# Optimization experiments

Hardware: AMD Instinct MI355X
Metric: run time of the kernel (lower is better)

Reference implementation:

```python
import jax, jax.numpy as jnp
import numpy as np

N_CHANNELS = 256
N_NEIGHBOURS = 262144
DIM = 3


def setup_inputs() -> dict:
    key = jax.random.key(0)
    k1, k2, k3 = jax.random.split(key, 3)
    h = jax.random.normal(k1, (N_CHANNELS, N_NEIGHBOURS), dtype=jnp.float32)
    rel_poss = jax.random.normal(k2, (DIM, N_NEIGHBOURS), dtype=jnp.float32)
    W = jax.random.normal(k3, (N_CHANNELS, N_CHANNELS), dtype=jnp.float32)
    return {"h": h, "rel_poss": rel_poss, "W": W}


def reference(h, rel_poss, W):
    # dists: [N], unit directions u: [dim, N]
    dists = jnp.linalg.norm(rel_poss, axis=0)
    u = rel_poss / dists
    # radial basis e_rbf(x, n, c=2) = (2/2)**0.5 * sin(n*x)/x = sin(n*x)/x, n = 1..K
    n = jnp.arange(1, N_CHANNELS + 1, dtype=h.dtype)
    radial_emb = jnp.sin(n[:, None] * dists[None, :]) / dists[None, :]  # [K, N]
    # channel-mixed features
    hp = W @ h  # [K, N]
    # per-neighbour: radial * feature scalar times rank-2 outer product u u^T, summed over neighbours
    m = radial_emb * hp  # [K, N]
    A = jnp.einsum('ki,di,ei->kde', m, u, u)  # [K, dim, dim]
    return A
```

## Files before the change

kernel.cpp:

```cpp
#include <hip/hip_runtime.h>
#include <hip/hip_bf16.h>

#define NCH      256
#define NNB      262144
#define BN       64
#define NTILES   (NNB / BN)
#define NB       256
#define ITPB     (NTILES / NB)
#define NENT     (NCH * 6)

typedef __bf16        bf16x8 __attribute__((ext_vector_type(8)));
typedef float         f32x4  __attribute__((ext_vector_type(4)));
typedef unsigned int  u32x4  __attribute__((ext_vector_type(4)));
typedef unsigned int  u32x2  __attribute__((ext_vector_type(2)));
typedef short         v4s    __attribute__((ext_vector_type(4)));

union FragU  { u32x4 u; bf16x8 b; };
union Frag2U { u32x2 u; v4s    s; };

__device__ __forceinline__ unsigned pk2(float lo, float hi) {
    union { __hip_bfloat162 h2; unsigned u; } cv;
    cv.h2 = __float22bfloat162_rn(make_float2(lo, hi));
    return cv.u;
}

__device__ __forceinline__ const float* uni_ptr(const float* p) {
    unsigned long long u = (unsigned long long)p;
    unsigned lo = __builtin_amdgcn_readfirstlane((unsigned)u);
    unsigned hi = __builtin_amdgcn_readfirstlane((unsigned)(u >> 32));
    return (const float*)(((unsigned long long)hi << 32) | lo);
}

#define LBAR() do {                                                  \
    asm volatile("s_waitcnt lgkmcnt(0)" ::: "memory");               \
    __builtin_amdgcn_sched_barrier(0);                               \
    __builtin_amdgcn_s_barrier();                                    \
    __builtin_amdgcn_sched_barrier(0);                               \
} while (0)

#define ITER(P, CUR, NXT, TILE_EXPR)                                               \
{                                                                                  \
    const int tile = (TILE_EXPR);                                                  \
    const int tn1  = tile + NB;                                                    \
    const int tn2  = tile + 2 * NB;                                                \
    {                      \
        const int lt = (tn2 < NTILES) ? tn2 : tile;                                \
        const unsigned ii = (unsigned)(lt * BN) + (unsigned)c;                     \
        NXT[0] = rp[ii];                                                           \
        NXT[1] = rp[(size_t)NNB + ii];                                             \
        NXT[2] = rp[2 * (size_t)NNB + ii];                                         \
    }                                                                              \
    __builtin_amdgcn_sched_barrier(0);                                             \
                      \
    _Pragma("unroll")                                                              \
    for (int cb = 0; cb < 4; ++cb) {                                               \
        const int colb = cb * 16;                                                  \
        Frag2U gf;                                                                 \
        gf.u = *(const u32x2*)((const char*)gT[P] +                                \
               (((unsigned)(il * 128 + (colb + q * 4) * 2)) ^                      \
                (((unsigned)(il & 7)) << 3)));                                     \
        f32x4 hpA = {0.f, 0.f, 0.f, 0.f}, hpB = {0.f, 0.f, 0.f, 0.f};              \
        const unsigned rb = (unsigned)((colb + il) * 512);                         \
        const unsigned sw = ((unsigned)(il & 7)) << 4;                             \
        _Pragma("unroll")                                                          \
        for (int jb = 0; jb < 8; jb += 2) {                                        \
            FragU f0, f1;                                                          \
            f0.u = *(const u32x4*)((const char*)htile[P] +                         \
                   ((rb + (unsigned)(jb * 64 + q * 16)) ^ sw));                    \
            f1.u = *(const u32x4*)((const char*)htile[P] +                         \
                   ((rb + (unsigned)((jb + 1) * 64 + q * 16)) ^ sw));              \
            hpA = __builtin_amdgcn_mfma_f32_16x16x32_bf16(f0.b, wf[jb].b, hpA, 0, 0, 0);     \
            hpB = __builtin_amdgcn_mfma_f32_16x16x32_bf16(f1.b, wf[jb + 1].b, hpB, 0, 0, 0); \
        }                                                                          \
        f32x4 d4 = *(const f32x4*)&dtab[P][0][colb + q * 4];                       \
        f32x4 i4 = *(const f32x4*)&dtab[P][1][colb + q * 4];                       \
        float m0 = __sinf(fk * d4[0]) * i4[0] * (hpA[0] + hpB[0]);                 \
        float m1 = __sinf(fk * d4[1]) * i4[1] * (hpA[1] + hpB[1]);                 \
        float m2 = __sinf(fk * d4[2]) * i4[2] * (hpA[2] + hpB[2]);                 \
        float m3 = __sinf(fk * d4[3]) * i4[3] * (hpA[3] + hpB[3]);                 \
        Frag2U af;                                                                 \
        af.u[0] = pk2(m0, m1);                                                     \
        af.u[1] = pk2(m2, m3);                                                     \
        acc = __builtin_amdgcn_mfma_f32_16x16x16bf16_1k(af.s, gf.s, acc, 0, 0, 0); \
    }                                                                              \
    __builtin_amdgcn_sched_barrier(0);                                             \
              \
    if (tn1 < NTILES) {                                                            \
        u32x4 w0, w1;                                                              \
        w0[0] = pk2(hv[0], hv[1]);   w0[1] = pk2(hv[2], hv[3]);                    \
        w0[2] = pk2(hv[4], hv[5]);   w0[3] = pk2(hv[6], hv[7]);                    \
        w1[0] = pk2(hv[8], hv[9]);   w1[1] = pk2(hv[10], hv[11]);                  \
        w1[2] = pk2(hv[12], hv[13]); w1[3] = pk2(hv[14], hv[15]);                  \
        const unsigned swc = ((unsigned)(c & 7)) << 4;                             \
        *(u32x4*)((char*)htile[(P) ^ 1] +                                          \
                  (((unsigned)(c * 512 + wave * 32)) ^ swc)) = w0;                 \
        *(u32x4*)((char*)htile[(P) ^ 1] +                                          \
                  (((unsigned)(c * 512 + wave * 32 + 16)) ^ swc)) = w1;            \
        float dd = sqrtf(CUR[0] * CUR[0] + CUR[1] * CUR[1] + CUR[2] * CUR[2]);     \
        float iv = 1.0f / dd;                                                      \
        if (t < 64) {                                                              \
            dtab[(P) ^ 1][0][c] = dd;                                              \
            dtab[(P) ^ 1][1][c] = iv;                                              \
            float i2 = iv * iv;                                                    \
            float gg[6] = { CUR[0] * CUR[0] * i2, CUR[0] * CUR[1] * i2,            \
                            CUR[0] * CUR[2] * i2, CUR[1] * CUR[1] * i2,            \
                            CUR[1] * CUR[2] * i2, CUR[2] * CUR[2] * i2 };          \
            _Pragma("unroll")                                                      \
            for (int de = 0; de < 6; ++de) {                                       \
                unsigned off = ((unsigned)(de * 128 + c * 2)) ^                    \
                               (((unsigned)de) << 3);                              \
                *(unsigned short*)((char*)gT[(P) ^ 1] + off) =                     \
                    (unsigned short)(pk2(gg[de], 0.f) & 0xffffu);                  \
            }                                                                      \
        }                                                                          \
        const int lt2 = (tn2 < NTILES) ? tn2 : tile;                               \
        const unsigned ii2 = (unsigned)(lt2 * BN) + (unsigned)c;                   \
        _Pragma("unroll")                                                          \
        for (int j = 0; j < 16; ++j) hv[j] = hwb[(size_t)j * NNB + ii2];           \
    }                                                                              \
    LBAR();                                                                        \
}

__global__ __launch_bounds__(1024, 1) void create_As_k1(
        const float* __restrict__ h, const float* __restrict__ rp,
        const float* __restrict__ W, float* __restrict__ ws)
{
    __shared__ unsigned short htile[2][BN * NCH];
    __shared__ unsigned short gT[2][16 * BN];
    __shared__ __align__(16) float dtab[2][2][BN];

    const int t    = threadIdx.x;
    const int wave = t >> 6;
    const int il   = t & 15;
    const int q    = (t >> 4) & 3;
    const int c    = t & 63;
    const int k0   = wave * 16;
    const float fk = (float)(k0 + il + 1);

    ((unsigned*)gT)[t] = 0u;

    FragU wf[8];
    {
        const float* wr = W + (size_t)(k0 + il) * NCH + q * 8;
        #pragma unroll
        for (int jb = 0; jb < 8; ++jb) {
            f32x4 a = *(const f32x4*)(wr + jb * 32);
            f32x4 b = *(const f32x4*)(wr + jb * 32 + 4);
            wf[jb].u[0] = pk2(a[0], a[1]);
            wf[jb].u[1] = pk2(a[2], a[3]);
            wf[jb].u[2] = pk2(b[0], b[1]);
            wf[jb].u[3] = pk2(b[2], b[3]);
        }
    }

    f32x4 acc = {0.f, 0.f, 0.f, 0.f};

    const float* hwb = uni_ptr(h + (size_t)(wave * 16) * NNB);

    float hv[16];
    float pA[3], pB[3];

    const int tile0 = blockIdx.x;

    __syncthreads();

    {
        const unsigned ii = (unsigned)(tile0 * BN) + (unsigned)c;
        pB[0] = rp[ii]; pB[1] = rp[(size_t)NNB + ii]; pB[2] = rp[2 * (size_t)NNB + ii];
        #pragma unroll
        for (int j = 0; j < 16; ++j) hv[j] = hwb[(size_t)j * NNB + ii];

        u32x4 w0, w1;
        w0[0] = pk2(hv[0], hv[1]);   w0[1] = pk2(hv[2], hv[3]);
        w0[2] = pk2(hv[4], hv[5]);   w0[3] = pk2(hv[6], hv[7]);
        w1[0] = pk2(hv[8], hv[9]);   w1[1] = pk2(hv[10], hv[11]);
        w1[2] = pk2(hv[12], hv[13]); w1[3] = pk2(hv[14], hv[15]);
        const unsigned swc = ((unsigned)(c & 7)) << 4;
        *(u32x4*)((char*)htile[0] + (((unsigned)(c * 512 + wave * 32)) ^ swc)) = w0;
        *(u32x4*)((char*)htile[0] + (((unsigned)(c * 512 + wave * 32 + 16)) ^ swc)) = w1;

        float dd = sqrtf(pB[0] * pB[0] + pB[1] * pB[1] + pB[2] * pB[2]);
        float iv = 1.0f / dd;
        if (t < 64) {
            dtab[0][0][c] = dd; dtab[0][1][c] = iv;
            float i2 = iv * iv;
            float gg[6] = { pB[0] * pB[0] * i2, pB[0] * pB[1] * i2, pB[0] * pB[2] * i2,
                            pB[1] * pB[1] * i2, pB[1] * pB[2] * i2, pB[2] * pB[2] * i2 };
            #pragma unroll
            for (int de = 0; de < 6; ++de) {
                unsigned off = ((unsigned)(de * 128 + c * 2)) ^ (((unsigned)de) << 3);
                *(unsigned short*)((char*)gT[0] + off) =
                    (unsigned short)(pk2(gg[de], 0.f) & 0xffffu);
            }
        }
        const unsigned i1 = (unsigned)((tile0 + NB) * BN) + (unsigned)c;
        pA[0] = rp[i1]; pA[1] = rp[(size_t)NNB + i1]; pA[2] = rp[2 * (size_t)NNB + i1];
        #pragma unroll
        for (int j = 0; j < 16; ++j) hv[j] = hwb[(size_t)j * NNB + i1];
    }
    LBAR();

    #pragma unroll 1
    for (int it2 = 0; it2 < ITPB; it2 += 2) {
        const int tb = tile0 + it2 * NB;
        ITER(0, pA, pB, tb)
        ITER(1, pB, pA, tb + NB)
    }

    if (il < 6) {
        float* dst = ws + (size_t)blockIdx.x * NENT;
        #pragma unroll
        for (int r = 0; r < 4; ++r)
            dst[(k0 + q * 4 + r) * 6 + il] = acc[r];
    }
}

__global__ void create_As_k2(const float* __restrict__ ws, float* __restrict__ out)
{
    __shared__ float red[8][64];
    const int eb = blockIdx.x;
    const int w  = threadIdx.x >> 6;
    const int l  = threadIdx.x & 63;
    float s = 0.f;
    #pragma unroll 4
    for (int b = w; b < NB; b += 8)
        s += ws[(size_t)b * NENT + (unsigned)(eb * 64 + l)];
    red[w][l] = s;
    __syncthreads();
    if (w == 0) {
        float v = red[0][l] + red[1][l] + red[2][l] + red[3][l]
                + red[4][l] + red[5][l] + red[6][l] + red[7][l];
        const int e  = eb * 64 + l;
        const int k  = e / 6;
        const int m6 = e - k * 6;
        const int d  = (m6 < 3) ? 0 : ((m6 < 5) ? 1 : 2);
        const int e2 = (m6 < 3) ? m6 : ((m6 < 5) ? (m6 - 2) : 2);
        out[k * 9 + d * 3 + e2] = v;
        if (d != e2) out[k * 9 + e2 * 3 + d] = v;
    }
}

extern "C" void kernel_launch(void* const* d_in, const int* in_sizes, int n_in,
                              void* d_out, int out_size, void* d_ws, size_t ws_size,
                              hipStream_t stream)
{
    const float* h  = (const float*)d_in[0];
    const float* rp = (const float*)d_in[1];
    const float* W  = (const float*)d_in[2];
    float* out = (float*)d_out;
    float* ws  = (float*)d_ws;

    hipLaunchKernelGGL(create_As_k1, dim3(NB), dim3(1024), 0, stream, h, rp, W, ws);
    hipLaunchKernelGGL(create_As_k2, dim3(NENT / 64), dim3(512), 0, stream, ws, out);
}
```

Before: 76.88 us.

## Split waves into column halves covering two channel tiles each, reusing h fragments

Each wave pair now shares a 32-channel group and splits the 64-neighbour columns between the two waves. Each h fragment loaded from LDS feeds two MFMAs, one per 16-channel W tile, so LDS reads per MFMA are halved. The cost is twice the W fragment registers plus a second accumulator. Partial results from the two column halves are combined through a new shared array and an extra barrier before the workspace store.

```diff
diff --git a/kernel.cpp b/kernel.cpp
--- a/kernel.cpp
+++ b/kernel.cpp
@@ -51,37 +51,42 @@
         NXT[2] = rp[2 * (size_t)NNB + ii];                                         \
     }                                                                              \
     __builtin_amdgcn_sched_barrier(0);                                             \
-                      \
+                           \
     _Pragma("unroll")                                                              \
-    for (int cb = 0; cb < 4; ++cb) {                                               \
-        const int colb = cb * 16;                                                  \
+    for (int cb = 0; cb < 2; ++cb) {                                               \
+        const int colb = g * 32 + cb * 16;                                         \
         Frag2U gf;                                                                 \
         gf.u = *(const u32x2*)((const char*)gT[P] +                                \
                (((unsigned)(il * 128 + (colb + q * 4) * 2)) ^                      \
                 (((unsigned)(il & 7)) << 3)));                                     \
-        f32x4 hpA = {0.f, 0.f, 0.f, 0.f}, hpB = {0.f, 0.f, 0.f, 0.f};              \
+        f32x4 hp0 = {0.f, 0.f, 0.f, 0.f}, hp1 = {0.f, 0.f, 0.f, 0.f};              \
         const unsigned rb = (unsigned)((colb + il) * 512);                         \
         const unsigned sw = ((unsigned)(il & 7)) << 4;                             \
         _Pragma("unroll")                                                          \
-        for (int jb = 0; jb < 8; jb += 2) {                                        \
-            FragU f0, f1;                                                          \
+        for (int jb = 0; jb < 8; ++jb) {                                           \
+            FragU f0;                                                              \
             f0.u = *(const u32x4*)((const char*)htile[P] +                         \
                    ((rb + (unsigned)(jb * 64 + q * 16)) ^ sw));                    \
-            f1.u = *(const u32x4*)((const char*)htile[P] +                         \
-                   ((rb + (unsigned)((jb + 1) * 64 + q * 16)) ^ sw));              \
-            hpA = __builtin_amdgcn_mfma_f32_16x16x32_bf16(f0.b, wf[jb].b, hpA, 0, 0, 0);     \
-            hpB = __builtin_amdgcn_mfma_f32_16x16x32_bf16(f1.b, wf[jb + 1].b, hpB, 0, 0, 0); \
+            hp0 = __builtin_amdgcn_mfma_f32_16x16x32_bf16(f0.b, wf[0][jb].b, hp0, 0, 0, 0); \
+            hp1 = __builtin_amdgcn_mfma_f32_16x16x32_bf16(f0.b, wf[1][jb].b, hp1, 0, 0, 0); \
         }                                                                          \
         f32x4 d4 = *(const f32x4*)&dtab[P][0][colb + q * 4];                       \
         f32x4 i4 = *(const f32x4*)&dtab[P][1][colb + q * 4];                       \
-        float m0 = __sinf(fk * d4[0]) * i4[0] * (hpA[0] + hpB[0]);                 \
-        float m1 = __sinf(fk * d4[1]) * i4[1] * (hpA[1] + hpB[1]);                 \
-        float m2 = __sinf(fk * d4[2]) * i4[2] * (hpA[2] + hpB[2]);                 \
-        float m3 = __sinf(fk * d4[3]) * i4[3] * (hpA[3] + hpB[3]);                 \
-        Frag2U af;                                                                 \
-        af.u[0] = pk2(m0, m1);                                                     \
-        af.u[1] = pk2(m2, m3);                                                     \
-        acc = __builtin_amdgcn_mfma_f32_16x16x16bf16_1k(af.s, gf.s, acc, 0, 0, 0); \
+        Frag2U a0, a1;                                                             \
+        {                                                                          \
+            float m0 = __sinf(fk0 * d4[0]) * i4[0] * hp0[0];                       \
+            float m1 = __sinf(fk0 * d4[1]) * i4[1] * hp0[1];                       \
+            float m2 = __sinf(fk0 * d4[2]) * i4[2] * hp0[2];                       \
+            float m3 = __sinf(fk0 * d4[3]) * i4[3] * hp0[3];                       \
+            a0.u[0] = pk2(m0, m1); a0.u[1] = pk2(m2, m3);                          \
+            float n0 = __sinf(fk1 * d4[0]) * i4[0] * hp1[0];                       \
+            float n1 = __sinf(fk1 * d4[1]) * i4[1] * hp1[1];                       \
+            float n2 = __sinf(fk1 * d4[2]) * i4[2] * hp1[2];                       \
+            float n3 = __sinf(fk1 * d4[3]) * i4[3] * hp1[3];                       \
+            a1.u[0] = pk2(n0, n1); a1.u[1] = pk2(n2, n3);                          \
+        }                                                                          \
+        acc0 = __builtin_amdgcn_mfma_f32_16x16x16bf16_1k(a0.s, gf.s, acc0, 0, 0, 0); \
+        acc1 = __builtin_amdgcn_mfma_f32_16x16x16bf16_1k(a1.s, gf.s, acc1, 0, 0, 0); \
     }                                                                              \
     __builtin_amdgcn_sched_barrier(0);                                             \
               \
@@ -128,32 +133,37 @@
     __shared__ unsigned short htile[2][BN * NCH];
     __shared__ unsigned short gT[2][16 * BN];
     __shared__ __align__(16) float dtab[2][2][BN];
+    __shared__ float ared[NCH][8];
 
     const int t    = threadIdx.x;
     const int wave = t >> 6;
     const int il   = t & 15;
     const int q    = (t >> 4) & 3;
     const int c    = t & 63;
-    const int k0   = wave * 16;
-    const float fk = (float)(k0 + il + 1);
+    const int g    = wave & 1;
+    const int kg   = wave >> 1;
+    const float fk0 = (float)(kg * 32 + il + 1);
+    const float fk1 = fk0 + 16.0f;
 
     ((unsigned*)gT)[t] = 0u;
 
-    FragU wf[8];
-    {
-        const float* wr = W + (size_t)(k0 + il) * NCH + q * 8;
+    FragU wf[2][8];
+    #pragma unroll
+    for (int kt = 0; kt < 2; ++kt) {
+        const float* wr = W + (size_t)(kg * 32 + kt * 16 + il) * NCH + q * 8;
         #pragma unroll
         for (int jb = 0; jb < 8; ++jb) {
             f32x4 a = *(const f32x4*)(wr + jb * 32);
             f32x4 b = *(const f32x4*)(wr + jb * 32 + 4);
-            wf[jb].u[0] = pk2(a[0], a[1]);
-            wf[jb].u[1] = pk2(a[2], a[3]);
-            wf[jb].u[2] = pk2(b[0], b[1]);
-            wf[jb].u[3] = pk2(b[2], b[3]);
-        }
-    }
-
-    f32x4 acc = {0.f, 0.f, 0.f, 0.f};
+            wf[kt][jb].u[0] = pk2(a[0], a[1]);
+            wf[kt][jb].u[1] = pk2(a[2], a[3]);
+            wf[kt][jb].u[2] = pk2(b[0], b[1]);
+            wf[kt][jb].u[3] = pk2(b[2], b[3]);
+        }
+    }
+
+    f32x4 acc0 = {0.f, 0.f, 0.f, 0.f};
+    f32x4 acc1 = {0.f, 0.f, 0.f, 0.f};
 
     const float* hwb = uni_ptr(h + (size_t)(wave * 16) * NNB);
 
@@ -207,11 +217,23 @@
         ITER(1, pB, pA, tb + NB)
     }
 
-    if (il < 6) {
+    if (g == 0 && il < 6) {
+        #pragma unroll
+        for (int r = 0; r < 4; ++r) {
+            ared[kg * 32 + q * 4 + r][il]      = acc0[r];
+            ared[kg * 32 + 16 + q * 4 + r][il] = acc1[r];
+        }
+    }
+    __syncthreads();
+    if (g == 1 && il < 6) {
         float* dst = ws + (size_t)blockIdx.x * NENT;
         #pragma unroll
-        for (int r = 0; r < 4; ++r)
-            dst[(k0 + q * 4 + r) * 6 + il] = acc[r];
+        for (int r = 0; r < 4; ++r) {
+            const int ka = kg * 32 + q * 4 + r;
+            const int kb = ka + 16;
+            dst[ka * 6 + il] = ared[ka][il] + acc0[r];
+            dst[kb * 6 + il] = ared[kb][il] + acc1[r];
+        }
     }
 }
 
```

Result: slower. 179.3 us (+133.3%).
